# Performance work log

Hardware: AMD Instinct MI355X
Metric: run time of the kernel (lower is better)

Reference implementation:

```python
import jax, jax.numpy as jnp
import numpy as np

B, CIN, COUT = 4, 512, 64
T, H, W = 16, 32, 32


def conv1x1(x, w, b=None):
    # 1x1x1 Conv3d == per-voxel linear: w (out, in), x (b, in, t, h, w)
    y = jnp.einsum('oc,bcthw->bothw', w, x)
    if b is not None:
        y = y + b[None, :, None, None, None]
    return y


def setup_inputs() -> dict:
    key = jax.random.key(0)
    ks = jax.random.split(key, 9)
    def kaiming(k, fan_out_shape):
        out_c, in_c = fan_out_shape
        std = np.sqrt(2.0 / out_c)  # fan_out mode for 1x1x1 kernel
        return jax.random.normal(k, fan_out_shape, dtype=jnp.float32) * std
    c4, c8 = CIN // 4, CIN // 8
    return {
        'x': jax.random.normal(ks[0], (B, CIN, T, H, W), dtype=jnp.float32),
        'w_add1': kaiming(ks[1], (CIN, CIN)), 'b_add1': jnp.zeros((CIN,), jnp.float32),
        'w_add2': kaiming(ks[2], (CIN, CIN)), 'b_add2': jnp.zeros((CIN,), jnp.float32),
        'w_occ1': kaiming(ks[3], (c4, CIN)), 'b_occ1': jnp.zeros((c4,), jnp.float32),
        'w_occ2': kaiming(ks[4], (c8, c4)), 'b_occ2': jnp.zeros((c8,), jnp.float32),
        'w_occ3': kaiming(ks[5], (COUT, c8)),  # bias=False
    }


def reference(x, w_add1, b_add1, w_add2, b_add2, w_occ1, b_occ1, w_occ2, b_occ2, w_occ3):
    # feature_map = add_on_layer(x): conv -> relu -> conv
    feat = conv1x1(jax.nn.relu(conv1x1(x, w_add1, b_add1)), w_add2, b_add2)
    # occ_map = abs(occ(x)): conv -> relu -> conv -> relu -> conv(no bias)
    h = jax.nn.relu(conv1x1(x, w_occ1, b_occ1))
    h = jax.nn.relu(conv1x1(h, w_occ2, b_occ2))
    occ = jnp.abs(conv1x1(h, w_occ3))  # (B, COUT, T, H, W)
    # output with pool='avg': mean over spatial of occ[:, :, None] * feat[:, None]
    # == einsum contraction over T*H*W, avoiding the (B,COUT,CIN,T,H,W) intermediate
    S = T * H * W
    out = jnp.einsum('bothw,bcthw->boc', occ, feat) / S  # (B, COUT, CIN)
    return out
```

## Files before the change

### kernel.cpp

```cpp
#include <hip/hip_runtime.h>


#define S_TOT 16384

typedef __attribute__((ext_vector_type(8))) short bf8_t;
typedef __attribute__((ext_vector_type(4))) short s4_t;
typedef __attribute__((ext_vector_type(4))) float f4_t;

#define MFMA __builtin_amdgcn_mfma_f32_16x16x32_bf16

__device__ __forceinline__ short f2bf(float f) {
  union { float f; unsigned u; } v; v.f = f;
  unsigned u = v.u + 0x7FFFu + ((v.u >> 16) & 1u);
  return (short)(u >> 16);
}
__device__ __forceinline__ float bf2f(short s) {
  union { unsigned u; float f; } v;
  v.u = ((unsigned)(unsigned short)s) << 16;
  return v.f;
}

__device__ __forceinline__ void glds16(const void* g, void* l) {
  __builtin_amdgcn_global_load_lds(
      (const __attribute__((address_space(1))) void*)g,
      (__attribute__((address_space(3))) void*)l, 16, 0, 0);
}

__device__ __forceinline__ void stage_tile(const short* gbase, short* lds,
                                           int wv, int lane) {
#pragma unroll
  for (int i = 0; i < 4; ++i) {
    const int slot0 = wv * 256 + i * 64;
    const int c = slot0 >> 7;
    const int r = (slot0 & 127) + lane;
    glds16(gbase + (size_t)r * 512 + c * 8, lds + slot0 * 8);
  }
}

__global__ __launch_bounds__(256) void k_convert(
    const float* __restrict__ w1, const float* __restrict__ wo1,
    const float* __restrict__ wo2, const float* __restrict__ wo3,
    short* __restrict__ dst) {
  int i = blockIdx.x * 256 + threadIdx.x;
  float v;
  if (i < 262144) v = w1[i];
  else if (i < 327680) v = wo1[i - 262144];
  else if (i < 335872) v = wo2[i - 327680];
  else if (i < 339968) v = wo3[i - 335872];
  else return;
  dst[i] = f2bf(v);
}

__global__ __launch_bounds__(256) void k_transpose(
    const float* __restrict__ x, short* __restrict__ xT) {
  __shared__ float tls[64][65];
  const int sb = blockIdx.x, cb = blockIdx.y, b = blockIdx.z;
  const int t = threadIdx.x;
  {
    const int cr = t >> 2, ss = (t & 3) * 16;
    const float* src = x + ((size_t)b * 512 + cb * 64 + cr) * S_TOT + sb * 64 + ss;
    f4_t v0 = *(const f4_t*)(src);
    f4_t v1 = *(const f4_t*)(src + 4);
    f4_t v2 = *(const f4_t*)(src + 8);
    f4_t v3 = *(const f4_t*)(src + 12);
#pragma unroll
    for (int j = 0; j < 4; ++j) {
      tls[cr][ss + j]      = v0[j];
      tls[cr][ss + 4 + j]  = v1[j];
      tls[cr][ss + 8 + j]  = v2[j];
      tls[cr][ss + 12 + j] = v3[j];
    }
  }
  __syncthreads();
  {
    const int sr = t >> 2, cs = (t & 3) * 16;
    alignas(16) short tmp[16];
#pragma unroll
    for (int j = 0; j < 16; ++j) tmp[j] = f2bf(tls[cs + j][sr]);
    short* dst = xT + ((size_t)b * S_TOT + sb * 64 + sr) * 512 + cb * 64 + cs;
    *(bf8_t*)dst       = *(const bf8_t*)&tmp[0];
    *(bf8_t*)(dst + 8) = *(const bf8_t*)&tmp[8];
  }
}

__global__ __launch_bounds__(256) void k_occ(
    const short* __restrict__ xT, const short* __restrict__ wo1,
    const short* __restrict__ wo2, const short* __restrict__ wo3,
    const float* __restrict__ bo1, const float* __restrict__ bo2,
    short* __restrict__ occ) {
  __shared__ short smem[32768];
  short* xs  = smem;
  short* ws  = smem + 8192;
  short* h1s = smem + 16384;
  const int tile = blockIdx.x, b = blockIdx.y;
  const int s0 = tile * 128;
  const int t = threadIdx.x, lane = t & 63, wv = t >> 6;
  const int q = lane >> 4, li = lane & 15;
  const int mh = (wv & 1) * 64, nh = (wv >> 1) * 64;
  const short* xTb = xT + ((size_t)b * S_TOT + s0) * 512;
  const f4_t fz = {0.f, 0.f, 0.f, 0.f};

  f4_t acc[4][4];
#pragma unroll
  for (int i = 0; i < 4; ++i)
#pragma unroll
    for (int j = 0; j < 4; ++j) acc[i][j] = fz;

  for (int k0 = 0; k0 < 512; k0 += 64) {
    __syncthreads();
    stage_tile(xTb + k0, xs, wv, lane);
    stage_tile(wo1 + k0, ws, wv, lane);
    __syncthreads();
#pragma unroll
    for (int kk = 0; kk < 2; ++kk) {
      const int pl = (4 * kk + q) * 128;
      bf8_t a[4], bb[4];
#pragma unroll
      for (int ma = 0; ma < 4; ++ma)
        a[ma] = *(const bf8_t*)&ws[(pl + mh + 16 * ma + li) * 8];
#pragma unroll
      for (int nb = 0; nb < 4; ++nb)
        bb[nb] = *(const bf8_t*)&xs[(pl + nh + 16 * nb + li) * 8];
#pragma unroll
      for (int ma = 0; ma < 4; ++ma)
#pragma unroll
        for (int nb = 0; nb < 4; ++nb)
          acc[ma][nb] = MFMA(a[ma], bb[nb], acc[ma][nb], 0, 0, 0);
    }
  }
  __syncthreads();
#pragma unroll
  for (int ma = 0; ma < 4; ++ma) {
    const int c40 = mh + 16 * ma + 4 * q;
    f4_t bv = *(const f4_t*)(bo1 + c40);
#pragma unroll
    for (int nb = 0; nb < 4; ++nb) {
      const int sl = nh + 16 * nb + li;
      s4_t p;
#pragma unroll
      for (int r = 0; r < 4; ++r) p[r] = f2bf(fmaxf(acc[ma][nb][r] + bv[r], 0.0f));
      *(s4_t*)&h1s[((c40 >> 3) * 128 + sl) * 8 + (c40 & 7)] = p;
    }
  }
  __syncthreads();
  f4_t a2[4][2];
#pragma unroll
  for (int i = 0; i < 4; ++i) { a2[i][0] = fz; a2[i][1] = fz; }
#pragma unroll
  for (int kk = 0; kk < 4; ++kk) {
    const int pl = (4 * kk + q) * 128;
    bf8_t a[4], bb[2];
#pragma unroll
    for (int ma = 0; ma < 4; ++ma)
      a[ma] = *(const bf8_t*)(wo2 + (size_t)(16 * ma + li) * 128 + kk * 32 + q * 8);
#pragma unroll
    for (int nb = 0; nb < 2; ++nb)
      bb[nb] = *(const bf8_t*)&h1s[(pl + 32 * wv + 16 * nb + li) * 8];
#pragma unroll
    for (int ma = 0; ma < 4; ++ma)
#pragma unroll
      for (int nb = 0; nb < 2; ++nb)
        a2[ma][nb] = MFMA(a[ma], bb[nb], a2[ma][nb], 0, 0, 0);
  }
#pragma unroll
  for (int ma = 0; ma < 4; ++ma) {
    const int c80 = 16 * ma + 4 * q;
    f4_t bv = *(const f4_t*)(bo2 + c80);
#pragma unroll
    for (int nb = 0; nb < 2; ++nb) {
      const int sl = 32 * wv + 16 * nb + li;
      s4_t p;
#pragma unroll
      for (int r = 0; r < 4; ++r) p[r] = f2bf(fmaxf(a2[ma][nb][r] + bv[r], 0.0f));
      *(s4_t*)&xs[((c80 >> 3) * 128 + sl) * 8 + (c80 & 7)] = p;
    }
  }
  f4_t a3[4][2];
#pragma unroll
  for (int i = 0; i < 4; ++i) { a3[i][0] = fz; a3[i][1] = fz; }
#pragma unroll
  for (int kk = 0; kk < 2; ++kk) {
    const int pl = (4 * kk + q) * 128;
    bf8_t a[4], bb[2];
#pragma unroll
    for (int ma = 0; ma < 4; ++ma)
      a[ma] = *(const bf8_t*)(wo3 + (size_t)(16 * ma + li) * 64 + kk * 32 + q * 8);
#pragma unroll
    for (int nb = 0; nb < 2; ++nb)
      bb[nb] = *(const bf8_t*)&xs[(pl + 32 * wv + 16 * nb + li) * 8];
#pragma unroll
    for (int ma = 0; ma < 4; ++ma)
#pragma unroll
      for (int nb = 0; nb < 2; ++nb)
        a3[ma][nb] = MFMA(a[ma], bb[nb], a3[ma][nb], 0, 0, 0);
  }
#pragma unroll
  for (int ma = 0; ma < 4; ++ma)
#pragma unroll
    for (int nb = 0; nb < 2; ++nb) {
      const int o = 16 * ma + 4 * q;
      const int sgl = s0 + 32 * wv + 16 * nb + li;
#pragma unroll
      for (int r = 0; r < 4; ++r)
        occ[((size_t)(b * 64 + o + r)) * S_TOT + sgl] = f2bf(fabsf(a3[ma][nb][r]));
    }
}

__global__ __launch_bounds__(256) void k_feat(
    const short* __restrict__ xT, const short* __restrict__ w1,
    const float* __restrict__ b1, const short* __restrict__ occ,
    float* __restrict__ M) {
  __shared__ short smem[16384];
  short* xs  = smem;
  short* ws  = smem + 8192;
  short* r1s = smem;
  const int sg = blockIdx.x, cb = blockIdx.y, b = blockIdx.z;
  const int t = threadIdx.x, lane = t & 63, wv = t >> 6;
  const int q = lane >> 4, li = lane & 15;
  const int mh = (wv & 1) * 64, nh = (wv >> 1) * 64;
  const short* w1b = w1 + (size_t)(cb * 128) * 512;
  const f4_t fz = {0.f, 0.f, 0.f, 0.f};

  float biasv[4];
#pragma unroll
  for (int nb = 0; nb < 4; ++nb) biasv[nb] = b1[cb * 128 + nh + 16 * nb + li];

  f4_t macc[4][2];
#pragma unroll
  for (int i = 0; i < 4; ++i) { macc[i][0] = fz; macc[i][1] = fz; }

  for (int tt = 0; tt < 4; ++tt) {
    const int s_t = (sg * 4 + tt) * 128;
    const short* xTb = xT + ((size_t)b * S_TOT + s_t) * 512;
    f4_t acc[4][4];
#pragma unroll
    for (int i = 0; i < 4; ++i)
#pragma unroll
      for (int j = 0; j < 4; ++j) acc[i][j] = fz;

    for (int k0 = 0; k0 < 512; k0 += 64) {
      __syncthreads();
      stage_tile(xTb + k0, xs, wv, lane);
      stage_tile(w1b + k0, ws, wv, lane);
      __syncthreads();
#pragma unroll
      for (int kk = 0; kk < 2; ++kk) {
        const int pl = (4 * kk + q) * 128;
        bf8_t a[4], bb[4];
#pragma unroll
        for (int ma = 0; ma < 4; ++ma)
          a[ma] = *(const bf8_t*)&xs[(pl + mh + 16 * ma + li) * 8];
#pragma unroll
        for (int nb = 0; nb < 4; ++nb)
          bb[nb] = *(const bf8_t*)&ws[(pl + nh + 16 * nb + li) * 8];
#pragma unroll
        for (int ma = 0; ma < 4; ++ma)
#pragma unroll
          for (int nb = 0; nb < 4; ++nb)
            acc[ma][nb] = MFMA(a[ma], bb[nb], acc[ma][nb], 0, 0, 0);
      }
    }
    __syncthreads();
    const short* ob = occ + (size_t)b * 64 * S_TOT + s_t;
    bf8_t af[4][4];
#pragma unroll
    for (int kc = 0; kc < 4; ++kc)
#pragma unroll
      for (int ma = 0; ma < 4; ++ma)
        af[ma][kc] = *(const bf8_t*)(ob + (size_t)(16 * ma + li) * S_TOT +
                                     kc * 32 + q * 8);
#pragma unroll
    for (int ma = 0; ma < 4; ++ma) {
      const int sl0 = mh + 16 * ma + 4 * q;
#pragma unroll
      for (int nb = 0; nb < 4; ++nb) {
        const int jl = nh + 16 * nb + li;
        s4_t p;
#pragma unroll
        for (int r = 0; r < 4; ++r)
          p[r] = f2bf(fmaxf(acc[ma][nb][r] + biasv[nb], 0.0f));
        *(s4_t*)&r1s[((sl0 >> 3) * 128 + jl) * 8 + (sl0 & 7)] = p;
      }
    }
    __syncthreads();
#pragma unroll
    for (int kc = 0; kc < 4; ++kc) {
      const int pl = (4 * kc + q) * 128;
      bf8_t bb[2];
#pragma unroll
      for (int nb = 0; nb < 2; ++nb)
        bb[nb] = *(const bf8_t*)&r1s[(pl + 32 * wv + 16 * nb + li) * 8];
#pragma unroll
      for (int ma = 0; ma < 4; ++ma)
#pragma unroll
        for (int nb = 0; nb < 2; ++nb)
          macc[ma][nb] = MFMA(af[ma][kc], bb[nb], macc[ma][nb], 0, 0, 0);
    }
  }
#pragma unroll
  for (int ma = 0; ma < 4; ++ma)
#pragma unroll
    for (int nb = 0; nb < 2; ++nb) {
      const int jg = cb * 128 + 32 * wv + 16 * nb + li;
#pragma unroll
      for (int r = 0; r < 4; ++r) {
        const int o = 16 * ma + 4 * q + r;
        atomicAdd(&M[((size_t)b * 64 + o) * 512 + jg], macc[ma][nb][r]);
      }
    }
}

__global__ __launch_bounds__(256) void k_epi(
    const short* __restrict__ occ, const float* __restrict__ M,
    const float* __restrict__ w2, const float* __restrict__ b2,
    float* __restrict__ out) {
  __shared__ float mrow[512];
  __shared__ float red[4];
  const int o = blockIdx.x, b = blockIdx.y;
  const int t = threadIdx.x;
  const short* orow = occ + ((size_t)b * 64 + o) * S_TOT;
  float s = 0.0f;
  for (int i = t * 8; i < S_TOT; i += 2048) {
    bf8_t v = *(const bf8_t*)(orow + i);
#pragma unroll
    for (int k = 0; k < 8; ++k) s += bf2f(v[k]);
  }
#pragma unroll
  for (int off = 32; off > 0; off >>= 1) s += __shfl_down(s, off);
  if ((t & 63) == 0) red[t >> 6] = s;
  for (int i = t; i < 512; i += 256) mrow[i] = M[((size_t)b * 64 + o) * 512 + i];
  __syncthreads();
  const float so = red[0] + red[1] + red[2] + red[3];
  for (int c = t; c < 512; c += 256) {
    const float* wr = w2 + (size_t)c * 512;
    float a = 0.0f;
    for (int jj = 0; jj < 512; jj += 4) {
      f4_t wv = *(const f4_t*)(wr + jj);
      a += wv[0] * mrow[jj] + wv[1] * mrow[jj + 1] +
           wv[2] * mrow[jj + 2] + wv[3] * mrow[jj + 3];
    }
    out[((size_t)b * 64 + o) * 512 + c] = (a + so * b2[c]) * (1.0f / 16384.0f);
  }
}

extern "C" void kernel_launch(void* const* d_in, const int* in_sizes, int n_in,
                              void* d_out, int out_size, void* d_ws, size_t ws_size,
                              hipStream_t stream) {
  (void)in_sizes; (void)n_in; (void)out_size; (void)ws_size;
  const float* x      = (const float*)d_in[0];
  const float* w_add1 = (const float*)d_in[1];
  const float* b_add1 = (const float*)d_in[2];
  const float* w_add2 = (const float*)d_in[3];
  const float* b_add2 = (const float*)d_in[4];
  const float* w_occ1 = (const float*)d_in[5];
  const float* b_occ1 = (const float*)d_in[6];
  const float* w_occ2 = (const float*)d_in[7];
  const float* b_occ2 = (const float*)d_in[8];
  const float* w_occ3 = (const float*)d_in[9];

  char* ws = (char*)d_ws;
  short* xT  = (short*)(ws);
  short* wb  = (short*)(ws + 67108864);
  short* occ = (short*)(ws + 67788800);
  float* M   = (float*)(ws + 76177408);

  hipMemsetAsync(M, 0, 4 * 64 * 512 * sizeof(float), stream);
  k_convert<<<dim3(1328), dim3(256), 0, stream>>>(w_add1, w_occ1, w_occ2, w_occ3, wb);
  k_transpose<<<dim3(256, 8, 4), dim3(256), 0, stream>>>(x, xT);

  const short* wb1  = wb;
  const short* wbo1 = wb + 262144;
  const short* wbo2 = wb + 327680;
  const short* wbo3 = wb + 335872;
  k_occ<<<dim3(128, 4), dim3(256), 0, stream>>>(xT, wbo1, wbo2, wbo3,
                                                b_occ1, b_occ2, occ);
  k_feat<<<dim3(32, 4, 4), dim3(256), 0, stream>>>(xT, wb1, b_add1, occ, M);
  k_epi<<<dim3(64, 4), dim3(256), 0, stream>>>(occ, M, w_add2, b_add2,
                                               (float*)d_out);
}
```

Baseline: 416.6 us.

## Double-buffer LDS staging in GEMM kernels and fuse occupancy sum into occ kernel

Both the occ and feat kernels now prefetch the next K-slice of activations and weights into a second LDS buffer while computing on the current one, dropping one barrier per step. The feat kernel also prefetches the next spatial tile during the occ-weighted reduction. The per-channel occ sum is accumulated with wave reductions and atomics inside k_occ, so the epilogue no longer rereads occ. The epilogue is restructured into a 2D grid computing one output per thread. Doubling LDS in k_feat may reduce occupancy.

After: 449.1 us. +7.8%, slower.

```diff
diff --git a/kernel.cpp b/kernel.cpp
--- a/kernel.cpp
+++ b/kernel.cpp
@@ -13,11 +13,6 @@
   union { float f; unsigned u; } v; v.f = f;
   unsigned u = v.u + 0x7FFFu + ((v.u >> 16) & 1u);
   return (short)(u >> 16);
-}
-__device__ __forceinline__ float bf2f(short s) {
-  union { unsigned u; float f; } v;
-  v.u = ((unsigned)(unsigned short)s) << 16;
-  return v.f;
 }
 
 __device__ __forceinline__ void glds16(const void* g, void* l) {
@@ -35,6 +30,11 @@
     const int r = (slot0 & 127) + lane;
     glds16(gbase + (size_t)r * 512 + c * 8, lds + slot0 * 8);
   }
+}
+__device__ __forceinline__ void stage_pair(const short* gx, const short* gw,
+                                           short* buf, int wv, int lane) {
+  stage_tile(gx, buf, wv, lane);
+  stage_tile(gw, buf + 8192, wv, lane);
 }
 
 __global__ __launch_bounds__(256) void k_convert(
@@ -87,11 +87,12 @@
     const short* __restrict__ xT, const short* __restrict__ wo1,
     const short* __restrict__ wo2, const short* __restrict__ wo3,
     const float* __restrict__ bo1, const float* __restrict__ bo2,
-    short* __restrict__ occ) {
+    short* __restrict__ occ, float* __restrict__ sumocc) {
   __shared__ short smem[32768];
-  short* xs  = smem;
-  short* ws  = smem + 8192;
-  short* h1s = smem + 16384;
+  short* const buf0 = smem;
+  short* const buf1 = smem + 16384;
+  short* const h1s = buf0;
+  short* const h2s = buf1;
   const int tile = blockIdx.x, b = blockIdx.y;
   const int s0 = tile * 128;
   const int t = threadIdx.x, lane = t & 63, wv = t >> 6;
@@ -106,18 +107,22 @@
 #pragma unroll
     for (int j = 0; j < 4; ++j) acc[i][j] = fz;
 
-  for (int k0 = 0; k0 < 512; k0 += 64) {
+  stage_pair(xTb, wo1, buf1, wv, lane);
+  int cur = 1;
+  for (int i = 0; i < 8; ++i) {
     __syncthreads();
-    stage_tile(xTb + k0, xs, wv, lane);
-    stage_tile(wo1 + k0, ws, wv, lane);
-    __syncthreads();
+    if (i < 7)
+      stage_pair(xTb + (i + 1) * 64, wo1 + (i + 1) * 64,
+                 (cur ? buf0 : buf1), wv, lane);
+    const short* xs = cur ? buf1 : buf0;
+    const short* wsp = xs + 8192;
 #pragma unroll
     for (int kk = 0; kk < 2; ++kk) {
       const int pl = (4 * kk + q) * 128;
       bf8_t a[4], bb[4];
 #pragma unroll
       for (int ma = 0; ma < 4; ++ma)
-        a[ma] = *(const bf8_t*)&ws[(pl + mh + 16 * ma + li) * 8];
+        a[ma] = *(const bf8_t*)&wsp[(pl + mh + 16 * ma + li) * 8];
 #pragma unroll
       for (int nb = 0; nb < 4; ++nb)
         bb[nb] = *(const bf8_t*)&xs[(pl + nh + 16 * nb + li) * 8];
@@ -127,6 +132,7 @@
         for (int nb = 0; nb < 4; ++nb)
           acc[ma][nb] = MFMA(a[ma], bb[nb], acc[ma][nb], 0, 0, 0);
     }
+    cur ^= 1;
   }
   __syncthreads();
 #pragma unroll
@@ -172,7 +178,7 @@
       s4_t p;
 #pragma unroll
       for (int r = 0; r < 4; ++r) p[r] = f2bf(fmaxf(a2[ma][nb][r] + bv[r], 0.0f));
-      *(s4_t*)&xs[((c80 >> 3) * 128 + sl) * 8 + (c80 & 7)] = p;
+      *(s4_t*)&h2s[((c80 >> 3) * 128 + sl) * 8 + (c80 & 7)] = p;
     }
   }
   f4_t a3[4][2];
@@ -187,7 +193,7 @@
       a[ma] = *(const bf8_t*)(wo3 + (size_t)(16 * ma + li) * 64 + kk * 32 + q * 8);
 #pragma unroll
     for (int nb = 0; nb < 2; ++nb)
-      bb[nb] = *(const bf8_t*)&xs[(pl + 32 * wv + 16 * nb + li) * 8];
+      bb[nb] = *(const bf8_t*)&h2s[(pl + 32 * wv + 16 * nb + li) * 8];
 #pragma unroll
     for (int ma = 0; ma < 4; ++ma)
 #pragma unroll
@@ -203,6 +209,15 @@
 #pragma unroll
       for (int r = 0; r < 4; ++r)
         occ[((size_t)(b * 64 + o + r)) * S_TOT + sgl] = f2bf(fabsf(a3[ma][nb][r]));
+    }
+#pragma unroll
+  for (int ma = 0; ma < 4; ++ma)
+#pragma unroll
+    for (int r = 0; r < 4; ++r) {
+      float v = fabsf(a3[ma][0][r]) + fabsf(a3[ma][1][r]);
+#pragma unroll
+      for (int m = 1; m < 16; m <<= 1) v += __shfl_xor(v, m, 64);
+      if (li == 0) atomicAdd(&sumocc[b * 64 + 16 * ma + 4 * q + r], v);
     }
 }
 
@@ -210,10 +225,10 @@
     const short* __restrict__ xT, const short* __restrict__ w1,
     const float* __restrict__ b1, const short* __restrict__ occ,
     float* __restrict__ M) {
-  __shared__ short smem[16384];
-  short* xs  = smem;
-  short* ws  = smem + 8192;
-  short* r1s = smem;
+  __shared__ short smem[32768];
+  short* const buf0 = smem;
+  short* const buf1 = smem + 16384;
+  short* const r1s = buf0;
   const int sg = blockIdx.x, cb = blockIdx.y, b = blockIdx.z;
   const int t = threadIdx.x, lane = t & 63, wv = t >> 6;
   const int q = lane >> 4, li = lane & 15;
@@ -229,20 +244,25 @@
 #pragma unroll
   for (int i = 0; i < 4; ++i) { macc[i][0] = fz; macc[i][1] = fz; }
 
+  stage_pair(xT + ((size_t)b * S_TOT + sg * 512) * 512, w1b, buf1, wv, lane);
+
   for (int tt = 0; tt < 4; ++tt) {
-    const int s_t = (sg * 4 + tt) * 128;
-    const short* xTb = xT + ((size_t)b * S_TOT + s_t) * 512;
+    const int s_t = sg * 512 + tt * 128;
+    const short* xTt = xT + ((size_t)b * S_TOT + s_t) * 512;
     f4_t acc[4][4];
 #pragma unroll
     for (int i = 0; i < 4; ++i)
 #pragma unroll
       for (int j = 0; j < 4; ++j) acc[i][j] = fz;
 
-    for (int k0 = 0; k0 < 512; k0 += 64) {
+    int cur = 1;
+    for (int i = 0; i < 8; ++i) {
       __syncthreads();
-      stage_tile(xTb + k0, xs, wv, lane);
-      stage_tile(w1b + k0, ws, wv, lane);
-      __syncthreads();
+      if (i < 7)
+        stage_pair(xTt + (i + 1) * 64, w1b + (i + 1) * 64,
+                   (cur ? buf0 : buf1), wv, lane);
+      const short* xs = cur ? buf1 : buf0;
+      const short* wsp = xs + 8192;
 #pragma unroll
       for (int kk = 0; kk < 2; ++kk) {
         const int pl = (4 * kk + q) * 128;
@@ -252,23 +272,16 @@
           a[ma] = *(const bf8_t*)&xs[(pl + mh + 16 * ma + li) * 8];
 #pragma unroll
         for (int nb = 0; nb < 4; ++nb)
-          bb[nb] = *(const bf8_t*)&ws[(pl + nh + 16 * nb + li) * 8];
+          bb[nb] = *(const bf8_t*)&wsp[(pl + nh + 16 * nb + li) * 8];
 #pragma unroll
         for (int ma = 0; ma < 4; ++ma)
 #pragma unroll
           for (int nb = 0; nb < 4; ++nb)
             acc[ma][nb] = MFMA(a[ma], bb[nb], acc[ma][nb], 0, 0, 0);
       }
+      cur ^= 1;
     }
     __syncthreads();
-    const short* ob = occ + (size_t)b * 64 * S_TOT + s_t;
-    bf8_t af[4][4];
-#pragma unroll
-    for (int kc = 0; kc < 4; ++kc)
-#pragma unroll
-      for (int ma = 0; ma < 4; ++ma)
-        af[ma][kc] = *(const bf8_t*)(ob + (size_t)(16 * ma + li) * S_TOT +
-                                     kc * 32 + q * 8);
 #pragma unroll
     for (int ma = 0; ma < 4; ++ma) {
       const int sl0 = mh + 16 * ma + 4 * q;
@@ -283,6 +296,16 @@
       }
     }
     __syncthreads();
+    if (tt < 3)
+      stage_pair(xTt + (size_t)128 * 512, w1b, buf1, wv, lane);
+    const short* ob = occ + (size_t)b * 64 * S_TOT + s_t;
+    bf8_t af[4][4];
+#pragma unroll
+    for (int kc = 0; kc < 4; ++kc)
+#pragma unroll
+      for (int ma = 0; ma < 4; ++ma)
+        af[ma][kc] = *(const bf8_t*)(ob + (size_t)(16 * ma + li) * S_TOT +
+                                     kc * 32 + q * 8);
 #pragma unroll
     for (int kc = 0; kc < 4; ++kc) {
       const int pl = (4 * kc + q) * 128;
@@ -310,37 +333,24 @@
     }
 }
 
-__global__ __launch_bounds__(256) void k_epi(
-    const short* __restrict__ occ, const float* __restrict__ M,
+__global__ __launch_bounds__(256) void k_out(
+    const float* __restrict__ M, const float* __restrict__ sumocc,
     const float* __restrict__ w2, const float* __restrict__ b2,
     float* __restrict__ out) {
-  __shared__ float mrow[512];
-  __shared__ float red[4];
-  const int o = blockIdx.x, b = blockIdx.y;
+  const int cg = blockIdx.x, og = blockIdx.y, b = blockIdx.z;
   const int t = threadIdx.x;
-  const short* orow = occ + ((size_t)b * 64 + o) * S_TOT;
-  float s = 0.0f;
-  for (int i = t * 8; i < S_TOT; i += 2048) {
-    bf8_t v = *(const bf8_t*)(orow + i);
-#pragma unroll
-    for (int k = 0; k < 8; ++k) s += bf2f(v[k]);
-  }
-#pragma unroll
-  for (int off = 32; off > 0; off >>= 1) s += __shfl_down(s, off);
-  if ((t & 63) == 0) red[t >> 6] = s;
-  for (int i = t; i < 512; i += 256) mrow[i] = M[((size_t)b * 64 + o) * 512 + i];
-  __syncthreads();
-  const float so = red[0] + red[1] + red[2] + red[3];
-  for (int c = t; c < 512; c += 256) {
-    const float* wr = w2 + (size_t)c * 512;
-    float a = 0.0f;
-    for (int jj = 0; jj < 512; jj += 4) {
-      f4_t wv = *(const f4_t*)(wr + jj);
-      a += wv[0] * mrow[jj] + wv[1] * mrow[jj + 1] +
-           wv[2] * mrow[jj + 2] + wv[3] * mrow[jj + 3];
-    }
-    out[((size_t)b * 64 + o) * 512 + c] = (a + so * b2[c]) * (1.0f / 16384.0f);
-  }
+  const int o = og * 16 + (t >> 4);
+  const int c = cg * 16 + (t & 15);
+  const float* mr = M + ((size_t)b * 64 + o) * 512;
+  const float* wr = w2 + (size_t)c * 512;
+  float a = 0.0f;
+  for (int j = 0; j < 512; j += 4) {
+    f4_t mv = *(const f4_t*)(mr + j);
+    f4_t wv = *(const f4_t*)(wr + j);
+    a += mv[0] * wv[0] + mv[1] * wv[1] + mv[2] * wv[2] + mv[3] * wv[3];
+  }
+  out[((size_t)b * 64 + o) * 512 + c] =
+      (a + sumocc[b * 64 + o] * b2[c]) * (1.0f / 16384.0f);
 }
 
 extern "C" void kernel_launch(void* const* d_in, const int* in_sizes, int n_in,
@@ -359,12 +369,13 @@
   const float* w_occ3 = (const float*)d_in[9];
 
   char* ws = (char*)d_ws;
-  short* xT  = (short*)(ws);
-  short* wb  = (short*)(ws + 67108864);
-  short* occ = (short*)(ws + 67788800);
-  float* M   = (float*)(ws + 76177408);
-
-  hipMemsetAsync(M, 0, 4 * 64 * 512 * sizeof(float), stream);
+  short* xT      = (short*)(ws);
+  short* wb      = (short*)(ws + 67108864);
+  short* occ     = (short*)(ws + 67788800);
+  float* M       = (float*)(ws + 76177408);
+  float* sumocc  = (float*)(ws + 76701696);
+
+  hipMemsetAsync(M, 0, 524288 + 1024, stream);
   k_convert<<<dim3(1328), dim3(256), 0, stream>>>(w_add1, w_occ1, w_occ2, w_occ3, wb);
   k_transpose<<<dim3(256, 8, 4), dim3(256), 0, stream>>>(x, xT);
 
@@ -373,8 +384,8 @@
   const short* wbo2 = wb + 327680;
   const short* wbo3 = wb + 335872;
   k_occ<<<dim3(128, 4), dim3(256), 0, stream>>>(xT, wbo1, wbo2, wbo3,
-                                                b_occ1, b_occ2, occ);
+                                                b_occ1, b_occ2, occ, sumocc);
   k_feat<<<dim3(32, 4, 4), dim3(256), 0, stream>>>(xT, wb1, b_add1, occ, M);
-  k_epi<<<dim3(64, 4), dim3(256), 0, stream>>>(occ, M, w_add2, b_add2,
-                                               (float*)d_out);
-}
+  k_out<<<dim3(32, 4, 4), dim3(256), 0, stream>>>(M, sumocc, w_add2, b_add2,
+                                                  (float*)d_out);
+}
```
